# Kernel tuning notes

Measured on AMD Instinct MI355X. Metric: run time of the kernel, lower is better.

## Reference

```python
import jax, jax.numpy as jnp
import numpy as np

B, S, D, E, K = 4, 2048, 1024, 8, 2
EPS, W_THRES, TEMP = 1e-4, 0.1, 1.0


def setup_inputs() -> dict:
    key = jax.random.key(0)
    k1, k2, k3, k4, k5 = jax.random.split(key, 5)
    x = jax.random.normal(k1, (B, S, D), dtype=jnp.float32)
    gate_W = jax.random.normal(k2, (D, E), dtype=jnp.float32) * 0.02
    gate_b = jnp.zeros((E,), dtype=jnp.float32)
    expert_W = jax.random.normal(k3, (E, D, D), dtype=jnp.float32) * 0.02
    expert_b = jnp.zeros((E, D), dtype=jnp.float32)
    return {"x": x, "gate_W": gate_W, "gate_b": gate_b,
            "expert_W": expert_W, "expert_b": expert_b}


def reference(x, gate_W, gate_b, expert_W, expert_b):
    # Gating: linear -> temperature -> clamp-min(eps) -> softmax
    scores = jnp.maximum((x @ gate_W + gate_b) / TEMP, EPS)      # [B,S,E]
    p = jax.nn.softmax(scores, axis=-1)                           # [B,S,E]
    _, topk_idx = jax.lax.top_k(p, K)                             # [B,S,K]
    # boolean membership mask of selected experts
    topk_mask = jax.nn.one_hot(topk_idx, E, dtype=p.dtype).sum(-2) > 0  # [B,S,E]
    # weights: clamp-min(weight_thres), normalized by detached sum over selected
    w = jnp.maximum(p, W_THRES)                                   # [B,S,E]
    w_gather = jnp.take_along_axis(w, topk_idx, axis=-1)          # [B,S,K]
    total = jax.lax.stop_gradient(w_gather.sum(-1, keepdims=True))
    w = w / total
    comb = jnp.where(topk_mask, w, jnp.zeros_like(w))             # [B,S,E]
    # Dense equivalent of gather/expert/scatter loop (E small): each expert
    # is Linear(D, D); masked combine weights zero out unselected experts.
    y = jnp.einsum('bsd,edf->bsef', x, expert_W) + expert_b       # [B,S,E,D]
    out = jnp.einsum('bsef,bse->bsf', y, comb) / K                # [B,S,D]
    return out
```

## Files before the change

kernel.cpp:

```cpp
#include <hip/hip_runtime.h>
#include <stdint.h>

#define TOK 8192
#define DIM 1024
#define NE 8

typedef short bf16x8 __attribute__((ext_vector_type(8)));
typedef float f32x4 __attribute__((ext_vector_type(4)));

__device__ __forceinline__ unsigned short f2bf(float f) {
  unsigned int u = __float_as_uint(f);
  u += 0x7FFFu + ((u >> 16) & 1u);
  return (unsigned short)(u >> 16);
}

__device__ __forceinline__ void gl_lds16(const void* g, void* l) {
  __builtin_amdgcn_global_load_lds(
      (__attribute__((address_space(1))) unsigned int*)(g),
      (__attribute__((address_space(3))) unsigned int*)(l), 16, 0, 0);
}

__global__ void zero_cnt(int* cnt) {
  if (threadIdx.x < NE) cnt[threadIdx.x] = 0;
}

__global__ __launch_bounds__(256) void gate_kernel(
    const float* __restrict__ x, const float* __restrict__ gW,
    const float* __restrict__ gb, unsigned short* __restrict__ xb,
    int* __restrict__ eSel, float* __restrict__ wSel)
{
  const int wave = threadIdx.x >> 6;
  const int lane = threadIdx.x & 63;
  const int t = blockIdx.x * 4 + wave;
  const float4* xrow = (const float4*)(x + (size_t)t * DIM);
  ushort4* xbrow = (ushort4*)(xb + (size_t)t * DIM);

  double acc[NE];
#pragma unroll
  for (int e = 0; e < NE; ++e) acc[e] = 0.0;

#pragma unroll
  for (int i = 0; i < 4; ++i) {
    const int j = i * 64 + lane;
    float4 v = xrow[j];
    ushort4 pk;
    pk.x = f2bf(v.x); pk.y = f2bf(v.y); pk.z = f2bf(v.z); pk.w = f2bf(v.w);
    xbrow[j] = pk;
    const float* g = gW + (size_t)j * 4 * NE;
    float xv[4] = {v.x, v.y, v.z, v.w};
#pragma unroll
    for (int c = 0; c < 4; ++c) {
#pragma unroll
      for (int e = 0; e < NE; ++e)
        acc[e] += (double)xv[c] * (double)g[c * NE + e];
    }
  }
#pragma unroll
  for (int off = 32; off > 0; off >>= 1) {
#pragma unroll
    for (int e = 0; e < NE; ++e)
      acc[e] += __shfl_xor(acc[e], off, 64);
  }

  if (lane == 0) {
    double s[NE];
#pragma unroll
    for (int e = 0; e < NE; ++e) {
      s[e] = acc[e] + (double)gb[e];
      if (s[e] < 1e-4) s[e] = 1e-4;
    }
    double m = s[0];
    for (int e = 1; e < NE; ++e) if (s[e] > m) m = s[e];
    double p[NE], Z = 0.0;
    for (int e = 0; e < NE; ++e) { p[e] = exp(s[e] - m); Z += p[e]; }
    int e0 = 0;
    for (int e = 1; e < NE; ++e) if (s[e] > s[e0]) e0 = e;
    int e1 = (e0 == 0) ? 1 : 0;
    for (int e = 0; e < NE; ++e) if (e != e0 && s[e] > s[e1]) e1 = e;
    double w0 = p[e0] / Z; if (w0 < 0.1) w0 = 0.1;
    double w1 = p[e1] / Z; if (w1 < 0.1) w1 = 0.1;
    const double inv = 0.5 / (w0 + w1);
    eSel[t * 2 + 0] = e0;
    eSel[t * 2 + 1] = e1;
    wSel[t * 2 + 0] = (float)(w0 * inv);
    wSel[t * 2 + 1] = (float)(w1 * inv);
  }
}

__global__ __launch_bounds__(256) void scatter_kernel(
    const int* __restrict__ eSel, const float* __restrict__ wSel,
    int* __restrict__ cnt, int* __restrict__ listTok, float* __restrict__ listW)
{
  __shared__ int lcnt[NE];
  __shared__ int base[NE];
  const int tid = threadIdx.x;
  if (tid < NE) lcnt[tid] = 0;
  __syncthreads();

  const int t = blockIdx.x * 256 + tid;
  const int e0 = eSel[t * 2 + 0];
  const int e1 = eSel[t * 2 + 1];
  const float w0 = wSel[t * 2 + 0];
  const float w1 = wSel[t * 2 + 1];
  const int l0 = atomicAdd(&lcnt[e0], 1);
  const int l1 = atomicAdd(&lcnt[e1], 1);
  __syncthreads();
  if (tid < NE) base[tid] = atomicAdd(&cnt[tid], lcnt[tid]);
  __syncthreads();

  const int p0 = base[e0] + l0;
  listTok[e0 * TOK + p0] = t * 2 + 0;
  listW [e0 * TOK + p0] = w0;
  const int p1 = base[e1] + l1;
  listTok[e1 * TOK + p1] = t * 2 + 1;
  listW [e1 * TOK + p1] = w1;
}

__global__ __launch_bounds__(256) void transpose_w(
    const float* __restrict__ W, unsigned short* __restrict__ Wt)
{
  __shared__ float tile[32][33];
  const int e = blockIdx.z;
  const int d0 = blockIdx.y * 32, f0 = blockIdx.x * 32;
  const int tx = threadIdx.x & 31, ty = threadIdx.x >> 5;
  const float* src = W + ((size_t)e * DIM + d0) * DIM + f0;
#pragma unroll
  for (int r = ty; r < 32; r += 8)
    tile[r][tx] = src[(size_t)r * DIM + tx];
  __syncthreads();
  unsigned short* dst = Wt + ((size_t)e * DIM + f0) * DIM + d0;
#pragma unroll
  for (int r = ty; r < 32; r += 8)
    dst[(size_t)r * DIM + tx] = f2bf(tile[tx][r]);
}

__global__ void build_desc(const int* __restrict__ cnt, int* __restrict__ tiles)
{
  if (threadIdx.x == 0 && blockIdx.x == 0) {
    int n = 0;
    for (int e = 0; e < NE; ++e) {
      int c = cnt[e];
      for (int r = 0; r < c; r += 128) {
        tiles[1 + n * 3] = e;
        tiles[2 + n * 3] = r;
        tiles[3 + n * 3] = (c - r < 128) ? (c - r) : 128;
        ++n;
      }
    }
    tiles[0] = n;
  }
}

__global__ __launch_bounds__(256) void moe_gemm(
    const unsigned short* __restrict__ xb, const unsigned short* __restrict__ Wt,
    const float* __restrict__ eb, const int* __restrict__ tiles,
    const int* __restrict__ listTok, const float* __restrict__ listW,
    float* __restrict__ yslot)
{
  const int dId = blockIdx.x >> 3;
  const int cT  = blockIdx.x & 7;
  if (dId >= tiles[0]) return;
  const int e    = tiles[1 + dId * 3];
  const int r0   = tiles[2 + dId * 3];
  const int rows = tiles[3 + dId * 3];

  __shared__ __align__(16) unsigned short As[128 * 32];
  __shared__ __align__(16) unsigned short Bs[128 * 32];
  __shared__ int   tid_s[128];
  __shared__ float w_s[128];

  const int tid = threadIdx.x;
  if (tid < 128) {
    if (tid < rows) {
      tid_s[tid] = listTok[e * TOK + r0 + tid];
      w_s[tid]   = listW [e * TOK + r0 + tid];
    } else {
      tid_s[tid] = 0;
      w_s[tid]   = 0.0f;
    }
  }
  __syncthreads();

  const int w    = tid >> 6;
  const int lane = tid & 63;
  const int kq   = lane & 3;
  const int rA0  = w * 32 + (lane >> 2);
  const int rA1  = rA0 + 16;
  const unsigned short* srcA0 = xb + (size_t)(tid_s[rA0] >> 1) * DIM + kq * 8;
  const unsigned short* srcA1 = xb + (size_t)(tid_s[rA1] >> 1) * DIM + kq * 8;
  const unsigned short* srcB0 = Wt + ((size_t)e * DIM + cT * 128 + rA0) * DIM + kq * 8;
  const unsigned short* srcB1 = Wt + ((size_t)e * DIM + cT * 128 + rA1) * DIM + kq * 8;
  unsigned short* ldsA = &As[w * 1024];
  unsigned short* ldsB = &Bs[w * 1024];

  const int wr = w >> 1, wc = w & 1;
  const int mrow = lane & 15;
  const int koff = (lane >> 4) * 8;

  f32x4 acc[4][4];
#pragma unroll
  for (int i = 0; i < 4; ++i)
#pragma unroll
    for (int j = 0; j < 4; ++j)
      acc[i][j] = {0.f, 0.f, 0.f, 0.f};

  for (int kc = 0; kc < DIM / 32; ++kc) {
    const int k0 = kc * 32;
    __syncthreads();
    gl_lds16(srcA0 + k0, ldsA);
    gl_lds16(srcA1 + k0, ldsA + 512);
    gl_lds16(srcB0 + k0, ldsB);
    gl_lds16(srcB1 + k0, ldsB + 512);
    __syncthreads();
    bf16x8 af[4], bfr[4];
#pragma unroll
    for (int mt = 0; mt < 4; ++mt)
      af[mt] = *(const bf16x8*)&As[(wr * 64 + mt * 16 + mrow) * 32 + koff];
#pragma unroll
    for (int nt = 0; nt < 4; ++nt)
      bfr[nt] = *(const bf16x8*)&Bs[(wc * 64 + nt * 16 + mrow) * 32 + koff];
#pragma unroll
    for (int mt = 0; mt < 4; ++mt)
#pragma unroll
      for (int nt = 0; nt < 4; ++nt)
        acc[mt][nt] = __builtin_amdgcn_mfma_f32_16x16x32_bf16(
            af[mt], bfr[nt], acc[mt][nt], 0, 0, 0);
  }

  const int colBase = cT * 128 + wc * 64 + mrow;
  float bias[4];
#pragma unroll
  for (int nt = 0; nt < 4; ++nt)
    bias[nt] = eb[(size_t)e * DIM + colBase + nt * 16];
#pragma unroll
  for (int mt = 0; mt < 4; ++mt) {
#pragma unroll
    for (int r = 0; r < 4; ++r) {
      const int rloc = wr * 64 + mt * 16 + (lane >> 4) * 4 + r;
      if (rloc < rows) {
        const int tk    = tid_s[rloc];
        const float wgt = w_s[rloc];
        float* dst = yslot + ((size_t)(tk & 1) * TOK + (size_t)(tk >> 1)) * DIM;
#pragma unroll
        for (int nt = 0; nt < 4; ++nt)
          dst[colBase + nt * 16] = wgt * (acc[mt][nt][r] + bias[nt]);
      }
    }
  }
}

__global__ __launch_bounds__(256) void combine(
    const float4* __restrict__ y0, const float4* __restrict__ y1,
    float4* __restrict__ out)
{
  const size_t i = (size_t)blockIdx.x * 256 + threadIdx.x;
  float4 a = y0[i], b = y1[i];
  float4 o;
  o.x = a.x + b.x; o.y = a.y + b.y; o.z = a.z + b.z; o.w = a.w + b.w;
  out[i] = o;
}

extern "C" void kernel_launch(void* const* d_in, const int* in_sizes, int n_in,
                              void* d_out, int out_size, void* d_ws, size_t ws_size,
                              hipStream_t stream)
{
  const float* x  = (const float*)d_in[0];
  const float* gW = (const float*)d_in[1];
  const float* gb = (const float*)d_in[2];
  const float* eW = (const float*)d_in[3];
  const float* eb = (const float*)d_in[4];
  float* out = (float*)d_out;

  char* p = (char*)d_ws;
  unsigned short* xb = (unsigned short*)p;  p += (size_t)TOK * DIM * 2;
  unsigned short* Wt = (unsigned short*)p;  p += (size_t)NE * DIM * DIM * 2;
  float* yslot = (float*)p;                 p += (size_t)2 * TOK * DIM * 4;
  int* cnt = (int*)p;                       p += 256;
  int* listTok = (int*)p;                   p += (size_t)NE * TOK * 4;
  float* listW = (float*)p;                 p += (size_t)NE * TOK * 4;
  int* tiles = (int*)p;                     p += 4096;

  int*   eSel = (int*)yslot;
  float* wSel = (float*)(yslot + TOK * 2);

  zero_cnt<<<1, 64, 0, stream>>>(cnt);
  gate_kernel<<<TOK / 4, 256, 0, stream>>>(x, gW, gb, xb, eSel, wSel);
  scatter_kernel<<<TOK / 256, 256, 0, stream>>>(eSel, wSel, cnt, listTok, listW);
  transpose_w<<<dim3(32, 32, 8), 256, 0, stream>>>(eW, Wt);
  build_desc<<<1, 64, 0, stream>>>(cnt, tiles);
  moe_gemm<<<136 * 8, 256, 0, stream>>>(xb, Wt, eb, tiles, listTok, listW, yslot);
  combine<<<TOK * DIM / 4 / 256, 256, 0, stream>>>(
      (const float4*)yslot, (const float4*)yslot + (size_t)TOK * DIM / 4, (float4*)out);
}
```

Before: 236.0 us.

## Load expert weight fragments directly to registers with prefetch, swizzle A tile in LDS

Expert weight (B) fragments are no longer staged through shared memory. Each lane now reads its bf16x8 fragments straight from global memory into registers, prefetching the next k-chunk during the current MFMA step. The A tile still goes through LDS, but its 16-byte chunks are XOR-swizzled on write and read to reduce bank conflicts. This cuts LDS traffic and frees shared memory, at the cost of more register pressure and uncoalesced global loads for B, which two warps in the same row now fetch redundantly.

```diff
diff --git a/kernel.cpp b/kernel.cpp
--- a/kernel.cpp
+++ b/kernel.cpp
@@ -165,7 +165,6 @@
   const int rows = tiles[3 + dId * 3];
 
   __shared__ __align__(16) unsigned short As[128 * 32];
-  __shared__ __align__(16) unsigned short Bs[128 * 32];
   __shared__ int   tid_s[128];
   __shared__ float w_s[128];
 
@@ -183,19 +182,22 @@
 
   const int w    = tid >> 6;
   const int lane = tid & 63;
-  const int kq   = lane & 3;
+  const int qsrc = (lane & 3) ^ ((lane >> 3) & 3);
   const int rA0  = w * 32 + (lane >> 2);
   const int rA1  = rA0 + 16;
-  const unsigned short* srcA0 = xb + (size_t)(tid_s[rA0] >> 1) * DIM + kq * 8;
-  const unsigned short* srcA1 = xb + (size_t)(tid_s[rA1] >> 1) * DIM + kq * 8;
-  const unsigned short* srcB0 = Wt + ((size_t)e * DIM + cT * 128 + rA0) * DIM + kq * 8;
-  const unsigned short* srcB1 = Wt + ((size_t)e * DIM + cT * 128 + rA1) * DIM + kq * 8;
+  const unsigned short* srcA0 = xb + (size_t)(tid_s[rA0] >> 1) * DIM + qsrc * 8;
+  const unsigned short* srcA1 = xb + (size_t)(tid_s[rA1] >> 1) * DIM + qsrc * 8;
   unsigned short* ldsA = &As[w * 1024];
-  unsigned short* ldsB = &Bs[w * 1024];
 
   const int wr = w >> 1, wc = w & 1;
   const int mrow = lane & 15;
-  const int koff = (lane >> 4) * 8;
+  const int qg   = lane >> 4;
+  const int qsA  = (qg ^ ((mrow >> 1) & 3)) * 8;
+
+  const unsigned short* pB[4];
+#pragma unroll
+  for (int nt = 0; nt < 4; ++nt)
+    pB[nt] = Wt + ((size_t)e * DIM + cT * 128 + wc * 64 + nt * 16 + mrow) * DIM + qg * 8;
 
   f32x4 acc[4][4];
 #pragma unroll
@@ -204,27 +206,34 @@
     for (int j = 0; j < 4; ++j)
       acc[i][j] = {0.f, 0.f, 0.f, 0.f};
 
+  bf16x8 bcur[4], bnext[4];
+#pragma unroll
+  for (int nt = 0; nt < 4; ++nt)
+    bcur[nt] = *(const bf16x8*)(pB[nt]);
+
   for (int kc = 0; kc < DIM / 32; ++kc) {
     const int k0 = kc * 32;
+    const int kn = ((kc + 1) & 31) * 32;
+#pragma unroll
+    for (int nt = 0; nt < 4; ++nt)
+      bnext[nt] = *(const bf16x8*)(pB[nt] + kn);
     __syncthreads();
     gl_lds16(srcA0 + k0, ldsA);
     gl_lds16(srcA1 + k0, ldsA + 512);
-    gl_lds16(srcB0 + k0, ldsB);
-    gl_lds16(srcB1 + k0, ldsB + 512);
     __syncthreads();
-    bf16x8 af[4], bfr[4];
+    bf16x8 af[4];
 #pragma unroll
     for (int mt = 0; mt < 4; ++mt)
-      af[mt] = *(const bf16x8*)&As[(wr * 64 + mt * 16 + mrow) * 32 + koff];
-#pragma unroll
-    for (int nt = 0; nt < 4; ++nt)
-      bfr[nt] = *(const bf16x8*)&Bs[(wc * 64 + nt * 16 + mrow) * 32 + koff];
+      af[mt] = *(const bf16x8*)&As[(wr * 64 + mt * 16 + mrow) * 32 + qsA];
 #pragma unroll
     for (int mt = 0; mt < 4; ++mt)
 #pragma unroll
       for (int nt = 0; nt < 4; ++nt)
         acc[mt][nt] = __builtin_amdgcn_mfma_f32_16x16x32_bf16(
-            af[mt], bfr[nt], acc[mt][nt], 0, 0, 0);
+            af[mt], bcur[nt], acc[mt][nt], 0, 0, 0);
+#pragma unroll
+    for (int nt = 0; nt < 4; ++nt)
+      bcur[nt] = bnext[nt];
   }
 
   const int colBase = cT * 128 + wc * 64 + mrow;
```

Measured after the change: 281.1 us. +19.1%, slower.
